# Performance work log

Hardware: AMD Instinct MI355X
Metric: run time of the kernel (lower is better)

Reference implementation:

```python
import jax, jax.numpy as jnp
import numpy as np

D_MODEL = 96
D_STATE = 6
D_CONV = 9
D_INNER = 2 * D_MODEL          # expand = 2
DT_RANK = (D_MODEL + 15) // 16  # ceil(d_model/16) = 6
DIM_IN = 64
DIM_OUT = 64
BATCH = 16
SEQLEN = 4096


def setup_inputs() -> dict:
    key = jax.random.key(0)
    ks = jax.random.split(key, 12)
    def s(k, shape, scale=0.02):
        return jax.random.normal(k, shape, jnp.float32) * scale
    return {
        "x": jax.random.normal(ks[0], (BATCH, SEQLEN, D_MODEL), jnp.float32),
        # Mamba block params
        "in_proj_w": s(ks[1], (2 * D_INNER, D_MODEL)),
        "conv_w": s(ks[2], (D_INNER, D_CONV), 0.1),   # depthwise conv kernel
        "conv_b": jnp.zeros((D_INNER,), jnp.float32),
        "x_proj_w": s(ks[3], (DT_RANK + 2 * D_STATE, D_INNER)),
        "dt_proj_w": s(ks[4], (D_INNER, DT_RANK), 0.1),
        "dt_proj_b": s(ks[5], (D_INNER,), 0.1),
        "A_log": jnp.log(jnp.tile(jnp.arange(1, D_STATE + 1, dtype=jnp.float32), (D_INNER, 1))),
        "D_param": jnp.ones((D_INNER,), jnp.float32),
        "out_proj_w": s(ks[6], (D_MODEL, D_INNER)),
        "norm_w": jnp.ones((D_MODEL,), jnp.float32),  # RMSNorm weight
        # heads
        "out_fc_w": s(ks[7], (DIM_IN, D_MODEL)),
        "out_fc_b": jnp.zeros((DIM_IN,), jnp.float32),
        "mu_w": s(ks[8], (DIM_OUT, DIM_IN)),
        "mu_b": jnp.zeros((DIM_OUT,), jnp.float32),
        "sigma_w": s(ks[9], (DIM_OUT, DIM_IN)),
        "sigma_b": jnp.zeros((DIM_OUT,), jnp.float32),
    }


def _mamba_block(x, in_proj_w, conv_w, conv_b, x_proj_w, dt_proj_w, dt_proj_b,
                 A_log, D_param, out_proj_w):
    Bsz = x.shape[0]
    xz = jnp.einsum('bld,ed->ble', x, in_proj_w)          # (B,L,2*ED)
    xs, z = jnp.split(xz, 2, axis=-1)
    # causal depthwise conv1d (torch pads d_conv-1 both sides then trims right)
    xt = xs.transpose(0, 2, 1)                            # (B,ED,L)
    kern = conv_w[:, None, :]                             # (ED,1,K)
    xc = jax.lax.conv_general_dilated(xt, kern, window_strides=(1,),
                                      padding=[(D_CONV - 1, 0)],
                                      feature_group_count=D_INNER)
    xc = (xc + conv_b[None, :, None]).transpose(0, 2, 1)  # (B,L,ED)
    xc = jax.nn.silu(xc)
    dbc = jnp.einsum('ble,fe->blf', xc, x_proj_w)         # (B,L,dt_rank+2N)
    delta_r = dbc[..., :DT_RANK]
    Bm = dbc[..., DT_RANK:DT_RANK + D_STATE]              # (B,L,N)
    Cm = dbc[..., DT_RANK + D_STATE:]                     # (B,L,N)
    delta = jax.nn.softplus(jnp.einsum('blr,er->ble', delta_r, dt_proj_w) + dt_proj_b)
    A = -jnp.exp(A_log)                                   # (ED,N)
    deltaA = jnp.exp(delta[..., None] * A)                # (B,L,ED,N)
    BX = (delta * xc)[..., None] * Bm[:, :, None, :]      # (B,L,ED,N)

    def step(h, inputs):
        dA, bx = inputs
        h = dA * h + bx
        return h, h

    h0 = jnp.zeros((Bsz, D_INNER, D_STATE), x.dtype)
    _, hs = jax.lax.scan(step, h0, (deltaA.swapaxes(0, 1), BX.swapaxes(0, 1)))
    y = jnp.einsum('lben,bln->ble', hs, Cm)               # (B,L,ED)
    y = y + D_param * xc
    y = y * jax.nn.silu(z)
    return jnp.einsum('ble,de->bld', y, out_proj_w)       # (B,L,D)


def reference(x, in_proj_w, conv_w, conv_b, x_proj_w, dt_proj_w, dt_proj_b,
              A_log, D_param, out_proj_w, norm_w,
              out_fc_w, out_fc_b, mu_w, mu_b, sigma_w, sigma_b):
    # residual block: x + mixer(RMSNorm(x))   (dropout is identity at eval)
    h = x * jax.lax.rsqrt(jnp.mean(x * x, axis=-1, keepdims=True) + 1e-5) * norm_w
    out = x + _mamba_block(h, in_proj_w, conv_w, conv_b, x_proj_w,
                           dt_proj_w, dt_proj_b, A_log, D_param, out_proj_w)
    e = out.mean(axis=1)                                  # (B,D)
    feat = jax.nn.elu(jnp.tanh(e @ out_fc_w.T + out_fc_b))
    mu = feat @ mu_w.T + mu_b
    sigma = jax.nn.elu(feat @ sigma_w.T + sigma_b) + 1.0 + 1e-14
    return (feat, mu, sigma)
```

## Files before the change

### kernel.cpp

```cpp
#include <hip/hip_runtime.h>
#include <math.h>

#define BATCH 16
#define SEQLEN 4096
#define D_MODEL 96
#define D_STATE 6
#define D_CONV 9
#define D_INNER 192
#define DT_RANK 6
#define NPOS (BATCH * SEQLEN)

#define NC2 128
#define CT2 (SEQLEN / NC2)
#define NSEG 16
#define CPS (NC2 / NSEG)

#define OFF_XS    0L
#define OFF_Z     (OFF_XS   + (long)NPOS * 96)
#define OFF_OUT4  (OFF_Z    + (long)NPOS * 96)
#define OFF_SEG   (OFF_OUT4 + (long)BATCH * NC2 * 5 * 192 * 4)
#define OFF_XPART (OFF_SEG  + (long)BATCH * NSEG * 5 * 192 * 4)
#define OFF_XPB   (OFF_XPART + (long)(NPOS / 32) * 96)
#define OFF_WB16  (OFF_XPB  + 18 * 96)

typedef short v8s __attribute__((ext_vector_type(8)));
typedef float v4f __attribute__((ext_vector_type(4)));

__device__ __forceinline__ float silu_fast(float v) {
    return __fdividef(v, 1.0f + __expf(-v));
}
__device__ __forceinline__ float softplus_fast(float v) {
    return (v > 20.0f) ? v : __logf(1.0f + __expf(v));
}
__device__ __forceinline__ float eluf(float v) {
    return (v > 0.0f) ? v : expm1f(v);
}
__device__ __forceinline__ unsigned int pack_bf16(float a, float b) {
    unsigned int ua = __float_as_uint(a), ub = __float_as_uint(b);
    ua += 0x7FFFu + ((ua >> 16) & 1u);
    ub += 0x7FFFu + ((ub >> 16) & 1u);
    return (ua >> 16) | (ub & 0xFFFF0000u);
}
__device__ __forceinline__ unsigned short bf16h(float v) {
    unsigned int u = __float_as_uint(v);
    u += 0x7FFFu + ((u >> 16) & 1u);
    return (unsigned short)(u >> 16);
}
__device__ __forceinline__ float bf2f(unsigned short h) {
    return __uint_as_float(((unsigned int)h) << 16);
}

#define K0_W (384 * 48)
#define K0_X (18 * 96)
__global__ __launch_bounds__(256) void k0_pack(
    const float* __restrict__ W, const float* __restrict__ x_proj_w,
    unsigned int* __restrict__ wb16, unsigned int* __restrict__ xpb)
{
    int i = blockIdx.x * 256 + threadIdx.x;
    if (i < K0_W) {
        const float2 wv = *(const float2*)&W[2 * i];
        wb16[i] = pack_bf16(wv.x, wv.y);
    } else if (i < K0_W + K0_X) {
        int j = i - K0_W;
        const float2 wv = *(const float2*)&x_proj_w[2 * j];
        xpb[j] = pack_bf16(wv.x, wv.y);
    }
}

#define TP1 32
__global__ __launch_bounds__(256, 4) void k1_rmsnorm_inproj(
    const float* __restrict__ x, const unsigned short* __restrict__ wb16,
    const float* __restrict__ norm_w,
    unsigned short* __restrict__ xs, unsigned short* __restrict__ z,
    float* __restrict__ xpart)
{
    __shared__ float hRow[TP1 * 100];
    __shared__ unsigned int s_hA[TP1 * 52];
    __shared__ float s_part[TP1][8];
    __shared__ float s_scale[TP1];

    const int tid = threadIdx.x;
    const long p0 = (long)blockIdx.x * TP1;

    {
        const float4* x4 = (const float4*)&x[p0 * 96];
        for (int i = tid; i < TP1 * 24; i += 256) {
            int p = i / 24, dq = i - p * 24;
            *(float4*)&hRow[p * 100 + dq * 4] = x4[i];
        }
    }
    __syncthreads();

    {
        int p = tid >> 3, g = tid & 7;
        float ss = 0.0f;
        for (int d = g; d < 96; d += 8) { float v = hRow[p * 100 + d]; ss += v * v; }
        s_part[p][g] = ss;
    }
    __syncthreads();

    if (tid < TP1) {
        float ss = 0.0f;
#pragma unroll
        for (int g = 0; g < 8; g++) ss += s_part[tid][g];
        s_scale[tid] = 1.0f / sqrtf(ss / 96.0f + 1e-5f);
    } else if (tid < TP1 + 96) {
        int d = tid - TP1;
        float s = 0.0f;
        for (int p = 0; p < TP1; p++) s += hRow[p * 100 + d];
        xpart[(long)blockIdx.x * 96 + d] = s;
    }
    __syncthreads();

    {
        const float2* nw2 = (const float2*)norm_w;
        for (int i = tid; i < TP1 * 48; i += 256) {
            int p = i / 48, dp = i - p * 48;
            float sc = s_scale[p];
            float2 nv = nw2[dp];
            float v0 = hRow[p * 100 + 2 * dp]     * sc * nv.x;
            float v1 = hRow[p * 100 + 2 * dp + 1] * sc * nv.y;
            s_hA[p * 52 + dp] = pack_bf16(v0, v1);
        }
    }
    __syncthreads();

    const int wave = tid >> 6, lane = tid & 63;
    const int quad = lane >> 4, ln = lane & 15;
    const int n0 = wave * 96;

    v4f acc[2][6];
#pragma unroll
    for (int mt = 0; mt < 2; mt++)
#pragma unroll
        for (int nt = 0; nt < 6; nt++) acc[mt][nt] = (v4f){0.f, 0.f, 0.f, 0.f};

    for (int kc = 0; kc < 3; kc++) {
        v8s bfh[2];
#pragma unroll
        for (int mt = 0; mt < 2; mt++)
            bfh[mt] = *(const v8s*)&s_hA[(mt * 16 + ln) * 52 + kc * 16 + quad * 4];
#pragma unroll
        for (int nt = 0; nt < 6; nt++) {
            v8s aw = *(const v8s*)&wb16[(n0 + nt * 16 + ln) * 96 + kc * 32 + quad * 8];
            acc[0][nt] = __builtin_amdgcn_mfma_f32_16x16x32_bf16(aw, bfh[0], acc[0][nt], 0, 0, 0);
            acc[1][nt] = __builtin_amdgcn_mfma_f32_16x16x32_bf16(aw, bfh[1], acc[1][nt], 0, 0, 0);
        }
    }

    unsigned short* dst = (wave < 2) ? xs : z;
    const bool is_z = (wave >= 2);
    const int jb = (wave & 1) * 96;
#pragma unroll
    for (int mt = 0; mt < 2; mt++) {
        long pos = p0 + mt * 16 + ln;
#pragma unroll
        for (int nt = 0; nt < 6; nt++) {
            float f0 = acc[mt][nt][0], f1 = acc[mt][nt][1];
            float f2 = acc[mt][nt][2], f3 = acc[mt][nt][3];
            if (is_z) {
                f0 = silu_fast(f0); f1 = silu_fast(f1);
                f2 = silu_fast(f2); f3 = silu_fast(f3);
            }
            uint2 v;
            v.x = pack_bf16(f0, f1);
            v.y = pack_bf16(f2, f3);
            *(uint2*)&dst[pos * D_INNER + jb + nt * 16 + quad * 4] = v;
        }
    }
}

#define SXSTR 200
__global__ __launch_bounds__(192, 4) void k2f_conv_scan(
    const unsigned short* __restrict__ xs, const unsigned short* __restrict__ z,
    const float* __restrict__ conv_w, const float* __restrict__ conv_b,
    const unsigned short* __restrict__ xpb,
    const float* __restrict__ dt_w, const float* __restrict__ dt_b,
    const float* __restrict__ A_log, const float* __restrict__ D_param,
    float4* __restrict__ out4)
{
    __shared__ unsigned short sxc[CT2 * SXSTR];
    __shared__ float sMeta[CT2][20];
    const int e = threadIdx.x;
    const int c = blockIdx.x & (NC2 - 1);
    const int b = blockIdx.x >> 7;
    const int l0 = c * CT2;
    const long brow = (long)b * SEQLEN;

    float cw[D_CONV];
#pragma unroll
    for (int k = 0; k < D_CONV; k++) cw[k] = conv_w[e * D_CONV + k];
    const float cb = conv_b[e];
    float win[D_CONV];
#pragma unroll
    for (int k = 0; k < 8; k++) {
        int ll = l0 - 8 + k;
        win[k] = (ll >= 0) ? bf2f(xs[(brow + ll) * D_INNER + e]) : 0.0f;
    }
#pragma unroll
    for (int r = 0; r < CT2; r++) {
        win[8] = bf2f(xs[(brow + l0 + r) * D_INNER + e]);
        float s = cb;
#pragma unroll
        for (int k = 0; k < D_CONV; k++) s += win[k] * cw[k];
        sxc[r * SXSTR + e] = bf16h(silu_fast(s));
#pragma unroll
        for (int k = 0; k < 8; k++) win[k] = win[k + 1];
    }

    const unsigned short* zp = &z[(brow + l0) * D_INNER + e];
    float zv[CT2];
#pragma unroll
    for (int t = 0; t < CT2; t++) zv[t] = bf2f(zp[(long)t * D_INNER]);
    __syncthreads();

    {
        const int wave = e >> 6, lane = e & 63;
        const int quad = lane >> 4, ln = lane & 15;
        if (wave < 2) {
            const int mt = wave;
            const int r1 = (ln < 2) ? 16 + ln : 0;
            v4f dacc[2];
            dacc[0] = (v4f){0.f, 0.f, 0.f, 0.f};
            dacc[1] = (v4f){0.f, 0.f, 0.f, 0.f};
#pragma unroll
            for (int kc = 0; kc < 6; kc++) {
                v8s af  = *(const v8s*)&sxc[(mt * 16 + ln) * SXSTR + kc * 32 + quad * 8];
                v8s bf0 = *(const v8s*)&xpb[ln * 192 + kc * 32 + quad * 8];
                v8s bf1 = *(const v8s*)&xpb[r1 * 192 + kc * 32 + quad * 8];
                dacc[0] = __builtin_amdgcn_mfma_f32_16x16x32_bf16(af, bf0, dacc[0], 0, 0, 0);
                dacc[1] = __builtin_amdgcn_mfma_f32_16x16x32_bf16(af, bf1, dacc[1], 0, 0, 0);
            }
#pragma unroll
            for (int nt = 0; nt < 2; nt++) {
                int f = nt * 16 + ln;
                if (f < 18) {
                    int col = (f < 6) ? f : f + 2;
#pragma unroll
                    for (int r = 0; r < 4; r++)
                        sMeta[mt * 16 + quad * 4 + r][col] = dacc[nt][r];
                }
            }
        }
    }
    __syncthreads();

    float a[D_STATE];
#pragma unroll
    for (int n = 0; n < D_STATE; n++) a[n] = -__expf(A_log[e * D_STATE + n]);
    float dtw[DT_RANK];
#pragma unroll
    for (int q = 0; q < DT_RANK; q++) dtw[q] = dt_w[e * DT_RANK + q];
    const float dtb = dt_b[e];
    const float Dv = D_param[e];
    const float a0 = a[0];

    bool pok = true;
#pragma unroll
    for (int n = 1; n < D_STATE; n++)
        pok = pok && (fabsf(a[n] - (float)(n + 1) * a0)
                      <= 1e-4f * (float)(n + 1) * fabsf(a0));
    unsigned long long pmask = __ballot(pok);

    float S[D_STATE], G[D_STATE];
#pragma unroll
    for (int n = 0; n < D_STATE; n++) { S[n] = 0.0f; G[n] = 0.0f; }
    float ysum0 = 0.0f;

    if (pmask == 0xFFFFFFFFFFFFFFFFull) {
        float Pa = 1.0f;
#pragma unroll 2
        for (int t = 0; t < CT2; t++) {
            const float4* m4 = (const float4*)&sMeta[t][0];
            float4 m0 = m4[0], m1 = m4[1], mB0 = m4[2], mB1 = m4[3], mC = m4[4];
            float Bv[6] = {mB0.x, mB0.y, mB0.z, mB0.w, mB1.x, mB1.y};
            float Cv[6] = {mB1.z, mB1.w, mC.x, mC.y, mC.z, mC.w};
            float dr = dtb + m0.x * dtw[0] + m0.y * dtw[1] + m0.z * dtw[2]
                     + m0.w * dtw[3] + m1.x * dtw[4] + m1.y * dtw[5];
            float dl = softplus_fast(dr);
            float xv = bf2f(sxc[t * SXSTR + e]);
            float zw = zv[t];
            float dx = dl * xv;
            float y = Dv * xv;
            float E = __expf(dl * a0);
            Pa *= E;
            float dA = E;
            float w = zw * Pa;
#pragma unroll
            for (int n = 0; n < D_STATE; n++) {
                S[n] = dA * S[n] + dx * Bv[n];
                y += S[n] * Cv[n];
                G[n] += w * Cv[n];
                dA *= E;
                w *= Pa;
            }
            ysum0 += zw * y;
        }
        long ob = (long)(b * NC2 + c) * 5 * 192 + e;
        float P1 = Pa, P2 = P1 * Pa, P3 = P2 * Pa, P4 = P3 * Pa, P5 = P4 * Pa, P6 = P5 * Pa;
        float4 q0, q1, q2, q3, q4;
        q0.x=P1; q0.y=P2; q0.z=P3; q0.w=P4;
        q1.x=P5; q1.y=P6; q1.z=S[0]; q1.w=S[1];
        q2.x=S[2]; q2.y=S[3]; q2.z=S[4]; q2.w=S[5];
        q3.x=G[0]; q3.y=G[1]; q3.z=G[2]; q3.w=G[3];
        q4.x=G[4]; q4.y=G[5]; q4.z=ysum0; q4.w=0.0f;
        out4[ob          ] = q0;
        out4[ob + 192    ] = q1;
        out4[ob + 2 * 192] = q2;
        out4[ob + 3 * 192] = q3;
        out4[ob + 4 * 192] = q4;
    } else {
        float P[D_STATE];
#pragma unroll
        for (int n = 0; n < D_STATE; n++) P[n] = 1.0f;
#pragma unroll 2
        for (int t = 0; t < CT2; t++) {
            const float4* m4 = (const float4*)&sMeta[t][0];
            float4 m0 = m4[0], m1 = m4[1], mB0 = m4[2], mB1 = m4[3], mC = m4[4];
            float Bv[6] = {mB0.x, mB0.y, mB0.z, mB0.w, mB1.x, mB1.y};
            float Cv[6] = {mB1.z, mB1.w, mC.x, mC.y, mC.z, mC.w};
            float dr = dtb + m0.x * dtw[0] + m0.y * dtw[1] + m0.z * dtw[2]
                     + m0.w * dtw[3] + m1.x * dtw[4] + m1.y * dtw[5];
            float dl = softplus_fast(dr);
            float xv = bf2f(sxc[t * SXSTR + e]);
            float zw = zv[t];
            float dx = dl * xv;
            float y = Dv * xv;
#pragma unroll
            for (int n = 0; n < D_STATE; n++) {
                float dA = __expf(dl * a[n]);
                S[n] = dA * S[n] + dx * Bv[n];
                P[n] *= dA;
                y += S[n] * Cv[n];
                G[n] += zw * P[n] * Cv[n];
            }
            ysum0 += zw * y;
        }
        long ob = (long)(b * NC2 + c) * 5 * 192 + e;
        float4 q0, q1, q2, q3, q4;
        q0.x=P[0]; q0.y=P[1]; q0.z=P[2]; q0.w=P[3];
        q1.x=P[4]; q1.y=P[5]; q1.z=S[0]; q1.w=S[1];
        q2.x=S[2]; q2.y=S[3]; q2.z=S[4]; q2.w=S[5];
        q3.x=G[0]; q3.y=G[1]; q3.z=G[2]; q3.w=G[3];
        q4.x=G[4]; q4.y=G[5]; q4.z=ysum0; q4.w=0.0f;
        out4[ob          ] = q0;
        out4[ob + 192    ] = q1;
        out4[ob + 2 * 192] = q2;
        out4[ob + 3 * 192] = q3;
        out4[ob + 4 * 192] = q4;
    }
}

__global__ __launch_bounds__(192) void k4_seg(
    const float4* __restrict__ out4, float4* __restrict__ seg4)
{
    const int e = threadIdx.x;
    const int s = blockIdx.x & (NSEG - 1);
    const int b = blockIdx.x >> 4;

    float H[D_STATE], Gq[D_STATE], Pp[D_STATE];
#pragma unroll
    for (int n = 0; n < D_STATE; n++) { H[n] = 0.0f; Gq[n] = 0.0f; Pp[n] = 1.0f; }
    float yb = 0.0f;
#pragma unroll 2
    for (int cc = 0; cc < CPS; cc++) {
        int c = s * CPS + cc;
        long ob = (long)(b * NC2 + c) * 5 * 192 + e;
        float4 q0 = out4[ob];
        float4 q1 = out4[ob + 192];
        float4 q2 = out4[ob + 2 * 192];
        float4 q3 = out4[ob + 3 * 192];
        float4 q4 = out4[ob + 4 * 192];
        float Pv[6] = {q0.x, q0.y, q0.z, q0.w, q1.x, q1.y};
        float Sv[6] = {q1.z, q1.w, q2.x, q2.y, q2.z, q2.w};
        float Gv[6] = {q3.x, q3.y, q3.z, q3.w, q4.x, q4.y};
        float g = 0.0f;
#pragma unroll
        for (int n = 0; n < D_STATE; n++) g += Gv[n] * H[n];
        yb += q4.z + g;
#pragma unroll
        for (int n = 0; n < D_STATE; n++) {
            Gq[n] += Gv[n] * Pp[n];
            H[n] = Pv[n] * H[n] + Sv[n];
            Pp[n] *= Pv[n];
        }
    }
    long sb = (long)(b * NSEG + s) * 5 * 192 + e;
    float4 q0, q1, q2, q3, q4;
    q0.x=Pp[0]; q0.y=Pp[1]; q0.z=Pp[2]; q0.w=Pp[3];
    q1.x=Pp[4]; q1.y=Pp[5]; q1.z=H[0]; q1.w=H[1];
    q2.x=H[2]; q2.y=H[3]; q2.z=H[4]; q2.w=H[5];
    q3.x=Gq[0]; q3.y=Gq[1]; q3.z=Gq[2]; q3.w=Gq[3];
    q4.x=Gq[4]; q4.y=Gq[5]; q4.z=yb; q4.w=0.0f;
    seg4[sb          ] = q0;
    seg4[sb + 192    ] = q1;
    seg4[sb + 2 * 192] = q2;
    seg4[sb + 3 * 192] = q3;
    seg4[sb + 4 * 192] = q4;
}

__global__ __launch_bounds__(192) void k4_head(
    const float4* __restrict__ seg4, const float* __restrict__ xpart,
    const float* __restrict__ Wout,
    const float* __restrict__ fc_w, const float* __restrict__ fc_b,
    const float* __restrict__ mu_w, const float* __restrict__ mu_b,
    const float* __restrict__ sg_w, const float* __restrict__ sg_b,
    float* __restrict__ out)
{
    __shared__ float ybar[D_INNER];
    __shared__ float sxb[D_MODEL];
    __shared__ float evec[D_MODEL];
    __shared__ float feat_s[64];
    const int e = threadIdx.x;
    const int b = blockIdx.x;

    float H[D_STATE];
#pragma unroll
    for (int n = 0; n < D_STATE; n++) H[n] = 0.0f;
    float yb = 0.0f;
#pragma unroll 4
    for (int s = 0; s < NSEG; s++) {
        long ob = (long)(b * NSEG + s) * 5 * 192 + e;
        float4 q0 = seg4[ob];
        float4 q1 = seg4[ob + 192];
        float4 q2 = seg4[ob + 2 * 192];
        float4 q3 = seg4[ob + 3 * 192];
        float4 q4 = seg4[ob + 4 * 192];
        float Pv[6] = {q0.x, q0.y, q0.z, q0.w, q1.x, q1.y};
        float Sv[6] = {q1.z, q1.w, q2.x, q2.y, q2.z, q2.w};
        float Gv[6] = {q3.x, q3.y, q3.z, q3.w, q4.x, q4.y};
        float g = 0.0f;
#pragma unroll
        for (int n = 0; n < D_STATE; n++) g += Gv[n] * H[n];
        yb += q4.z + g;
#pragma unroll
        for (int n = 0; n < D_STATE; n++) H[n] = Pv[n] * H[n] + Sv[n];
    }
    ybar[e] = yb;

    if (e < D_MODEL) {
        const float* xp = &xpart[(long)b * 128 * 96 + e];
        float s = 0.0f;
        for (int t = 0; t < 128; t++) s += xp[t * 96];
        sxb[e] = s;
    }
    __syncthreads();

    if (e < D_MODEL) {
        float s = sxb[e];
        const float* wrow = &Wout[e * D_INNER];
        for (int e2 = 0; e2 < D_INNER; e2++) s += ybar[e2] * wrow[e2];
        evec[e] = s / (float)SEQLEN;
    }
    __syncthreads();

    if (e < 64) {
        float s = fc_b[e];
        const float* wrow = &fc_w[e * D_MODEL];
        for (int d = 0; d < D_MODEL; d++) s += evec[d] * wrow[d];
        float f = eluf(tanhf(s));
        feat_s[e] = f;
        out[b * 64 + e] = f;
    }
    __syncthreads();

    if (e < 64) {
        float smu = mu_b[e], ssg = sg_b[e];
        const float* mrow = &mu_w[e * 64];
        const float* srow = &sg_w[e * 64];
        for (int i = 0; i < 64; i++) {
            smu += feat_s[i] * mrow[i];
            ssg += feat_s[i] * srow[i];
        }
        out[1024 + b * 64 + e] = smu;
        out[2048 + b * 64 + e] = eluf(ssg) + 1.0f + 1e-14f;
    }
}

extern "C" void kernel_launch(void* const* d_in, const int* in_sizes, int n_in,
                              void* d_out, int out_size, void* d_ws, size_t ws_size,
                              hipStream_t stream) {
    const float* x         = (const float*)d_in[0];
    const float* in_proj_w = (const float*)d_in[1];
    const float* conv_w    = (const float*)d_in[2];
    const float* conv_b    = (const float*)d_in[3];
    const float* x_proj_w  = (const float*)d_in[4];
    const float* dt_proj_w = (const float*)d_in[5];
    const float* dt_proj_b = (const float*)d_in[6];
    const float* A_log     = (const float*)d_in[7];
    const float* D_param   = (const float*)d_in[8];
    const float* out_proj_w= (const float*)d_in[9];
    const float* norm_w    = (const float*)d_in[10];
    const float* out_fc_w  = (const float*)d_in[11];
    const float* out_fc_b  = (const float*)d_in[12];
    const float* mu_w      = (const float*)d_in[13];
    const float* mu_b      = (const float*)d_in[14];
    const float* sigma_w   = (const float*)d_in[15];
    const float* sigma_b   = (const float*)d_in[16];
    float* ws = (float*)d_ws;
    float* out = (float*)d_out;

    k0_pack<<<(K0_W + K0_X + 255) / 256, 256, 0, stream>>>(
        in_proj_w, x_proj_w,
        (unsigned int*)(ws + OFF_WB16), (unsigned int*)(ws + OFF_XPB));

    k1_rmsnorm_inproj<<<NPOS / TP1, 256, 0, stream>>>(
        x, (const unsigned short*)(ws + OFF_WB16), norm_w,
        (unsigned short*)(ws + OFF_XS), (unsigned short*)(ws + OFF_Z),
        ws + OFF_XPART);

    k2f_conv_scan<<<BATCH * NC2, 192, 0, stream>>>(
        (const unsigned short*)(ws + OFF_XS), (const unsigned short*)(ws + OFF_Z),
        conv_w, conv_b, (const unsigned short*)(ws + OFF_XPB),
        dt_proj_w, dt_proj_b, A_log, D_param,
        (float4*)(ws + OFF_OUT4));

    k4_seg<<<BATCH * NSEG, 192, 0, stream>>>(
        (const float4*)(ws + OFF_OUT4), (float4*)(ws + OFF_SEG));

    k4_head<<<BATCH, 192, 0, stream>>>(
        (const float4*)(ws + OFF_SEG), ws + OFF_XPART, out_proj_w,
        out_fc_w, out_fc_b, mu_w, mu_b, sigma_w, sigma_b, out);
}
```

Before: 195.1 us.

## Split conv+x_proj GEMM out of scan kernel into separate pre-pass kernel

Moves the depthwise causal conv, SiLU and x_proj MFMA GEMM out of the fused scan kernel into a new kernel that processes 64-position tiles and writes xc (bf16) and the dt/B/C projections (fp32) to workspace. The scan kernel then only loads these precomputed tiles into shared memory before the chunked scan. This shortens the per-block prologue of the scan kernel and removes its conv halo recompute. In exchange it adds an extra kernel launch and a global round trip for xc and the projection values.

```diff
diff --git a/kernel.cpp b/kernel.cpp
--- a/kernel.cpp
+++ b/kernel.cpp
@@ -22,6 +22,8 @@
 #define OFF_XPART (OFF_SEG  + (long)BATCH * NSEG * 5 * 192 * 4)
 #define OFF_XPB   (OFF_XPART + (long)(NPOS / 32) * 96)
 #define OFF_WB16  (OFF_XPB  + 18 * 96)
+#define OFF_XC    (OFF_WB16 + 384 * 48)
+#define OFF_DBC   (OFF_XC   + (long)NPOS * 96)
 
 typedef short v8s __attribute__((ext_vector_type(8)));
 typedef float v4f __attribute__((ext_vector_type(4)));
@@ -171,10 +173,81 @@
 }
 
 #define SXSTR 200
-__global__ __launch_bounds__(192, 4) void k2f_conv_scan(
-    const unsigned short* __restrict__ xs, const unsigned short* __restrict__ z,
+#define CVP 64
+__global__ __launch_bounds__(192, 4) void k15_convgemm(
+    const unsigned short* __restrict__ xs,
     const float* __restrict__ conv_w, const float* __restrict__ conv_b,
     const unsigned short* __restrict__ xpb,
+    unsigned short* __restrict__ xc, float* __restrict__ dbcw)
+{
+    __shared__ unsigned short sxk[CVP * SXSTR];
+    const int e = threadIdx.x;
+    const int s = blockIdx.x & 63;
+    const int b = blockIdx.x >> 6;
+    const int l0 = s * CVP;
+    const long brow = (long)b * SEQLEN;
+
+    float cw[D_CONV];
+#pragma unroll
+    for (int k = 0; k < D_CONV; k++) cw[k] = conv_w[e * D_CONV + k];
+    const float cb = conv_b[e];
+    float win[D_CONV];
+#pragma unroll
+    for (int k = 0; k < 8; k++) {
+        int ll = l0 - 8 + k;
+        win[k] = (ll >= 0) ? bf2f(xs[(brow + ll) * D_INNER + e]) : 0.0f;
+    }
+    const unsigned short* xp = &xs[(brow + l0) * D_INNER + e];
+    unsigned short* cp = &xc[(brow + l0) * D_INNER + e];
+#pragma unroll 8
+    for (int r = 0; r < CVP; r++) {
+        win[8] = bf2f(xp[(long)r * D_INNER]);
+        float sa = cb;
+#pragma unroll
+        for (int k = 0; k < D_CONV; k++) sa += win[k] * cw[k];
+        unsigned short h = bf16h(silu_fast(sa));
+        sxk[r * SXSTR + e] = h;
+        cp[(long)r * D_INNER] = h;
+#pragma unroll
+        for (int k = 0; k < 8; k++) win[k] = win[k + 1];
+    }
+    __syncthreads();
+
+    const int wave = e >> 6, lane = e & 63;
+    const int quad = lane >> 4, ln = lane & 15;
+    if (wave < 2) {
+        const int r1 = (ln < 2) ? 16 + ln : 0;
+#pragma unroll
+        for (int half = 0; half < 2; half++) {
+            const int mt = wave * 2 + half;
+            v4f dacc[2];
+            dacc[0] = (v4f){0.f, 0.f, 0.f, 0.f};
+            dacc[1] = (v4f){0.f, 0.f, 0.f, 0.f};
+#pragma unroll
+            for (int kc = 0; kc < 6; kc++) {
+                v8s af  = *(const v8s*)&sxk[(mt * 16 + ln) * SXSTR + kc * 32 + quad * 8];
+                v8s bf0 = *(const v8s*)&xpb[ln * 192 + kc * 32 + quad * 8];
+                v8s bf1 = *(const v8s*)&xpb[r1 * 192 + kc * 32 + quad * 8];
+                dacc[0] = __builtin_amdgcn_mfma_f32_16x16x32_bf16(af, bf0, dacc[0], 0, 0, 0);
+                dacc[1] = __builtin_amdgcn_mfma_f32_16x16x32_bf16(af, bf1, dacc[1], 0, 0, 0);
+            }
+#pragma unroll
+            for (int nt = 0; nt < 2; nt++) {
+                int f = nt * 16 + ln;
+                if (f < 18) {
+                    int col = (f < 6) ? f : f + 2;
+#pragma unroll
+                    for (int r = 0; r < 4; r++)
+                        dbcw[(brow + l0 + mt * 16 + quad * 4 + r) * 20 + col] = dacc[nt][r];
+                }
+            }
+        }
+    }
+}
+
+__global__ __launch_bounds__(192, 4) void k2s_scan(
+    const unsigned short* __restrict__ xc, const unsigned short* __restrict__ z,
+    const float* __restrict__ dbcw,
     const float* __restrict__ dt_w, const float* __restrict__ dt_b,
     const float* __restrict__ A_log, const float* __restrict__ D_param,
     float4* __restrict__ out4)
@@ -187,62 +260,25 @@
     const int l0 = c * CT2;
     const long brow = (long)b * SEQLEN;
 
-    float cw[D_CONV];
-#pragma unroll
-    for (int k = 0; k < D_CONV; k++) cw[k] = conv_w[e * D_CONV + k];
-    const float cb = conv_b[e];
-    float win[D_CONV];
-#pragma unroll
-    for (int k = 0; k < 8; k++) {
-        int ll = l0 - 8 + k;
-        win[k] = (ll >= 0) ? bf2f(xs[(brow + ll) * D_INNER + e]) : 0.0f;
-    }
-#pragma unroll
-    for (int r = 0; r < CT2; r++) {
-        win[8] = bf2f(xs[(brow + l0 + r) * D_INNER + e]);
-        float s = cb;
-#pragma unroll
-        for (int k = 0; k < D_CONV; k++) s += win[k] * cw[k];
-        sxc[r * SXSTR + e] = bf16h(silu_fast(s));
-#pragma unroll
-        for (int k = 0; k < 8; k++) win[k] = win[k + 1];
-    }
-
+    if (e < 160) {
+        int t = e / 5, q = e - t * 5;
+        *(float4*)&sMeta[t][q * 4] =
+            *(const float4*)&dbcw[(brow + l0 + t) * 20 + q * 4];
+    }
+    {
+        const unsigned short* src = &xc[(brow + l0) * D_INNER];
+#pragma unroll
+        for (int j = 0; j < 4; j++) {
+            int i = e + j * 192;
+            int row = i / 24, c8 = i - row * 24;
+            *(v8s*)&sxc[row * SXSTR + c8 * 8] =
+                *(const v8s*)&src[row * D_INNER + c8 * 8];
+        }
+    }
     const unsigned short* zp = &z[(brow + l0) * D_INNER + e];
     float zv[CT2];
 #pragma unroll
     for (int t = 0; t < CT2; t++) zv[t] = bf2f(zp[(long)t * D_INNER]);
-    __syncthreads();
-
-    {
-        const int wave = e >> 6, lane = e & 63;
-        const int quad = lane >> 4, ln = lane & 15;
-        if (wave < 2) {
-            const int mt = wave;
-            const int r1 = (ln < 2) ? 16 + ln : 0;
-            v4f dacc[2];
-            dacc[0] = (v4f){0.f, 0.f, 0.f, 0.f};
-            dacc[1] = (v4f){0.f, 0.f, 0.f, 0.f};
-#pragma unroll
-            for (int kc = 0; kc < 6; kc++) {
-                v8s af  = *(const v8s*)&sxc[(mt * 16 + ln) * SXSTR + kc * 32 + quad * 8];
-                v8s bf0 = *(const v8s*)&xpb[ln * 192 + kc * 32 + quad * 8];
-                v8s bf1 = *(const v8s*)&xpb[r1 * 192 + kc * 32 + quad * 8];
-                dacc[0] = __builtin_amdgcn_mfma_f32_16x16x32_bf16(af, bf0, dacc[0], 0, 0, 0);
-                dacc[1] = __builtin_amdgcn_mfma_f32_16x16x32_bf16(af, bf1, dacc[1], 0, 0, 0);
-            }
-#pragma unroll
-            for (int nt = 0; nt < 2; nt++) {
-                int f = nt * 16 + ln;
-                if (f < 18) {
-                    int col = (f < 6) ? f : f + 2;
-#pragma unroll
-                    for (int r = 0; r < 4; r++)
-                        sMeta[mt * 16 + quad * 4 + r][col] = dacc[nt][r];
-                }
-            }
-        }
-    }
     __syncthreads();
 
     float a[D_STATE];
@@ -509,9 +545,14 @@
         (unsigned short*)(ws + OFF_XS), (unsigned short*)(ws + OFF_Z),
         ws + OFF_XPART);
 
-    k2f_conv_scan<<<BATCH * NC2, 192, 0, stream>>>(
-        (const unsigned short*)(ws + OFF_XS), (const unsigned short*)(ws + OFF_Z),
-        conv_w, conv_b, (const unsigned short*)(ws + OFF_XPB),
+    k15_convgemm<<<BATCH * (SEQLEN / CVP), 192, 0, stream>>>(
+        (const unsigned short*)(ws + OFF_XS), conv_w, conv_b,
+        (const unsigned short*)(ws + OFF_XPB),
+        (unsigned short*)(ws + OFF_XC), ws + OFF_DBC);
+
+    k2s_scan<<<BATCH * NC2, 192, 0, stream>>>(
+        (const unsigned short*)(ws + OFF_XC), (const unsigned short*)(ws + OFF_Z),
+        ws + OFF_DBC,
         dt_proj_w, dt_proj_b, A_log, D_param,
         (float4*)(ws + OFF_OUT4));
 
```

After: 202.1 us. +3.6%, slower.

## Process two scan chunks per block with interleaved independent recurrences

Applied to the files above, without the earlier changes.

Each conv/scan block now handles two adjacent chunks instead of one, halving the grid. The two chunks' scan recurrences are interleaved in one loop to expose instruction-level parallelism across independent dependency chains. The conv window is shared across the chunks, which removes a redundant halo reload. The z values for both chunks are packed as bf16 pairs into one register array. In exchange it uses more registers and shared memory per block and launches fewer blocks, which may reduce occupancy or load balance.

```diff
diff --git a/kernel.cpp b/kernel.cpp
--- a/kernel.cpp
+++ b/kernel.cpp
@@ -12,6 +12,7 @@
 
 #define NC2 128
 #define CT2 (SEQLEN / NC2)
+#define CPB 2
 #define NSEG 16
 #define CPS (NC2 / NSEG)
 
@@ -179,12 +180,13 @@
     const float* __restrict__ A_log, const float* __restrict__ D_param,
     float4* __restrict__ out4)
 {
-    __shared__ unsigned short sxc[CT2 * SXSTR];
-    __shared__ float sMeta[CT2][20];
+    __shared__ unsigned short sxc[CPB * CT2 * SXSTR];
+    __shared__ float sMeta[CPB * CT2][20];
     const int e = threadIdx.x;
-    const int c = blockIdx.x & (NC2 - 1);
-    const int b = blockIdx.x >> 7;
-    const int l0 = c * CT2;
+    const int cidx = blockIdx.x & (NC2 / CPB - 1);
+    const int b = blockIdx.x >> 6;
+    const int c0 = cidx * CPB;
+    const int l0 = c0 * CT2;
     const long brow = (long)b * SEQLEN;
 
     float cw[D_CONV];
@@ -197,9 +199,10 @@
         int ll = l0 - 8 + k;
         win[k] = (ll >= 0) ? bf2f(xs[(brow + ll) * D_INNER + e]) : 0.0f;
     }
-#pragma unroll
-    for (int r = 0; r < CT2; r++) {
-        win[8] = bf2f(xs[(brow + l0 + r) * D_INNER + e]);
+    const unsigned short* xsp = &xs[(brow + l0) * D_INNER + e];
+#pragma unroll 8
+    for (int r = 0; r < CPB * CT2; r++) {
+        win[8] = bf2f(xsp[(long)r * D_INNER]);
         float s = cb;
 #pragma unroll
         for (int k = 0; k < D_CONV; k++) s += win[k] * cw[k];
@@ -209,36 +212,43 @@
     }
 
     const unsigned short* zp = &z[(brow + l0) * D_INNER + e];
-    float zv[CT2];
-#pragma unroll
-    for (int t = 0; t < CT2; t++) zv[t] = bf2f(zp[(long)t * D_INNER]);
+    unsigned int zq[CT2];
+#pragma unroll
+    for (int t = 0; t < CT2; t++) {
+        unsigned int lo = zp[(long)t * D_INNER];
+        unsigned int hi = zp[(long)(t + CT2) * D_INNER];
+        zq[t] = lo | (hi << 16);
+    }
     __syncthreads();
 
     {
         const int wave = e >> 6, lane = e & 63;
         const int quad = lane >> 4, ln = lane & 15;
         if (wave < 2) {
-            const int mt = wave;
             const int r1 = (ln < 2) ? 16 + ln : 0;
-            v4f dacc[2];
-            dacc[0] = (v4f){0.f, 0.f, 0.f, 0.f};
-            dacc[1] = (v4f){0.f, 0.f, 0.f, 0.f};
-#pragma unroll
-            for (int kc = 0; kc < 6; kc++) {
-                v8s af  = *(const v8s*)&sxc[(mt * 16 + ln) * SXSTR + kc * 32 + quad * 8];
-                v8s bf0 = *(const v8s*)&xpb[ln * 192 + kc * 32 + quad * 8];
-                v8s bf1 = *(const v8s*)&xpb[r1 * 192 + kc * 32 + quad * 8];
-                dacc[0] = __builtin_amdgcn_mfma_f32_16x16x32_bf16(af, bf0, dacc[0], 0, 0, 0);
-                dacc[1] = __builtin_amdgcn_mfma_f32_16x16x32_bf16(af, bf1, dacc[1], 0, 0, 0);
-            }
-#pragma unroll
-            for (int nt = 0; nt < 2; nt++) {
-                int f = nt * 16 + ln;
-                if (f < 18) {
-                    int col = (f < 6) ? f : f + 2;
-#pragma unroll
-                    for (int r = 0; r < 4; r++)
-                        sMeta[mt * 16 + quad * 4 + r][col] = dacc[nt][r];
+#pragma unroll
+            for (int half = 0; half < 2; half++) {
+                const int mt = wave * 2 + half;
+                v4f dacc[2];
+                dacc[0] = (v4f){0.f, 0.f, 0.f, 0.f};
+                dacc[1] = (v4f){0.f, 0.f, 0.f, 0.f};
+#pragma unroll
+                for (int kc = 0; kc < 6; kc++) {
+                    v8s af  = *(const v8s*)&sxc[(mt * 16 + ln) * SXSTR + kc * 32 + quad * 8];
+                    v8s bf0 = *(const v8s*)&xpb[ln * 192 + kc * 32 + quad * 8];
+                    v8s bf1 = *(const v8s*)&xpb[r1 * 192 + kc * 32 + quad * 8];
+                    dacc[0] = __builtin_amdgcn_mfma_f32_16x16x32_bf16(af, bf0, dacc[0], 0, 0, 0);
+                    dacc[1] = __builtin_amdgcn_mfma_f32_16x16x32_bf16(af, bf1, dacc[1], 0, 0, 0);
+                }
+#pragma unroll
+                for (int nt = 0; nt < 2; nt++) {
+                    int f = nt * 16 + ln;
+                    if (f < 18) {
+                        int col = (f < 6) ? f : f + 2;
+#pragma unroll
+                        for (int r = 0; r < 4; r++)
+                            sMeta[mt * 16 + quad * 4 + r][col] = dacc[nt][r];
+                    }
                 }
             }
         }
@@ -262,92 +272,141 @@
                       <= 1e-4f * (float)(n + 1) * fabsf(a0));
     unsigned long long pmask = __ballot(pok);
 
-    float S[D_STATE], G[D_STATE];
-#pragma unroll
-    for (int n = 0; n < D_STATE; n++) { S[n] = 0.0f; G[n] = 0.0f; }
-    float ysum0 = 0.0f;
-
     if (pmask == 0xFFFFFFFFFFFFFFFFull) {
-        float Pa = 1.0f;
-#pragma unroll 2
+        float SA[D_STATE], GA[D_STATE], SB[D_STATE], GB[D_STATE];
+#pragma unroll
+        for (int n = 0; n < D_STATE; n++) {
+            SA[n] = 0.0f; GA[n] = 0.0f; SB[n] = 0.0f; GB[n] = 0.0f;
+        }
+        float PaA = 1.0f, PaB = 1.0f, ysA = 0.0f, ysB = 0.0f;
         for (int t = 0; t < CT2; t++) {
-            const float4* m4 = (const float4*)&sMeta[t][0];
-            float4 m0 = m4[0], m1 = m4[1], mB0 = m4[2], mB1 = m4[3], mC = m4[4];
-            float Bv[6] = {mB0.x, mB0.y, mB0.z, mB0.w, mB1.x, mB1.y};
-            float Cv[6] = {mB1.z, mB1.w, mC.x, mC.y, mC.z, mC.w};
-            float dr = dtb + m0.x * dtw[0] + m0.y * dtw[1] + m0.z * dtw[2]
-                     + m0.w * dtw[3] + m1.x * dtw[4] + m1.y * dtw[5];
-            float dl = softplus_fast(dr);
-            float xv = bf2f(sxc[t * SXSTR + e]);
-            float zw = zv[t];
-            float dx = dl * xv;
-            float y = Dv * xv;
-            float E = __expf(dl * a0);
-            Pa *= E;
-            float dA = E;
-            float w = zw * Pa;
-#pragma unroll
-            for (int n = 0; n < D_STATE; n++) {
-                S[n] = dA * S[n] + dx * Bv[n];
-                y += S[n] * Cv[n];
-                G[n] += w * Cv[n];
-                dA *= E;
-                w *= Pa;
+            {
+                const float4* m4 = (const float4*)&sMeta[t][0];
+                float4 m0 = m4[0], m1 = m4[1], mB0 = m4[2], mB1 = m4[3], mC = m4[4];
+                float Bv[6] = {mB0.x, mB0.y, mB0.z, mB0.w, mB1.x, mB1.y};
+                float Cv[6] = {mB1.z, mB1.w, mC.x, mC.y, mC.z, mC.w};
+                float dr = dtb + m0.x * dtw[0] + m0.y * dtw[1] + m0.z * dtw[2]
+                         + m0.w * dtw[3] + m1.x * dtw[4] + m1.y * dtw[5];
+                float dl = softplus_fast(dr);
+                float xv = bf2f(sxc[t * SXSTR + e]);
+                float zw = __uint_as_float(zq[t] << 16);
+                float dx = dl * xv;
+                float y = Dv * xv;
+                float E = __expf(dl * a0);
+                PaA *= E;
+                float dA = E;
+                float w = zw * PaA;
+#pragma unroll
+                for (int n = 0; n < D_STATE; n++) {
+                    SA[n] = dA * SA[n] + dx * Bv[n];
+                    y += SA[n] * Cv[n];
+                    GA[n] += w * Cv[n];
+                    dA *= E;
+                    w *= PaA;
+                }
+                ysA += zw * y;
             }
-            ysum0 += zw * y;
-        }
-        long ob = (long)(b * NC2 + c) * 5 * 192 + e;
-        float P1 = Pa, P2 = P1 * Pa, P3 = P2 * Pa, P4 = P3 * Pa, P5 = P4 * Pa, P6 = P5 * Pa;
-        float4 q0, q1, q2, q3, q4;
-        q0.x=P1; q0.y=P2; q0.z=P3; q0.w=P4;
-        q1.x=P5; q1.y=P6; q1.z=S[0]; q1.w=S[1];
-        q2.x=S[2]; q2.y=S[3]; q2.z=S[4]; q2.w=S[5];
-        q3.x=G[0]; q3.y=G[1]; q3.z=G[2]; q3.w=G[3];
-        q4.x=G[4]; q4.y=G[5]; q4.z=ysum0; q4.w=0.0f;
-        out4[ob          ] = q0;
-        out4[ob + 192    ] = q1;
-        out4[ob + 2 * 192] = q2;
-        out4[ob + 3 * 192] = q3;
-        out4[ob + 4 * 192] = q4;
+            {
+                const float4* m4 = (const float4*)&sMeta[CT2 + t][0];
+                float4 m0 = m4[0], m1 = m4[1], mB0 = m4[2], mB1 = m4[3], mC = m4[4];
+                float Bv[6] = {mB0.x, mB0.y, mB0.z, mB0.w, mB1.x, mB1.y};
+                float Cv[6] = {mB1.z, mB1.w, mC.x, mC.y, mC.z, mC.w};
+                float dr = dtb + m0.x * dtw[0] + m0.y * dtw[1] + m0.z * dtw[2]
+                         + m0.w * dtw[3] + m1.x * dtw[4] + m1.y * dtw[5];
+                float dl = softplus_fast(dr);
+                float xv = bf2f(sxc[(CT2 + t) * SXSTR + e]);
+                float zw = __uint_as_float(zq[t] & 0xFFFF0000u);
+                float dx = dl * xv;
+                float y = Dv * xv;
+                float E = __expf(dl * a0);
+                PaB *= E;
+                float dA = E;
+                float w = zw * PaB;
+#pragma unroll
+                for (int n = 0; n < D_STATE; n++) {
+                    SB[n] = dA * SB[n] + dx * Bv[n];
+                    y += SB[n] * Cv[n];
+                    GB[n] += w * Cv[n];
+                    dA *= E;
+                    w *= PaB;
+                }
+                ysB += zw * y;
+            }
+        }
+        {
+            long ob = (long)(b * NC2 + c0) * 5 * 192 + e;
+            float Pa = PaA;
+            float P1 = Pa, P2 = P1 * Pa, P3 = P2 * Pa, P4 = P3 * Pa, P5 = P4 * Pa, P6 = P5 * Pa;
+            float4 q0, q1, q2, q3, q4;
+            q0.x=P1; q0.y=P2; q0.z=P3; q0.w=P4;
+            q1.x=P5; q1.y=P6; q1.z=SA[0]; q1.w=SA[1];
+            q2.x=SA[2]; q2.y=SA[3]; q2.z=SA[4]; q2.w=SA[5];
+            q3.x=GA[0]; q3.y=GA[1]; q3.z=GA[2]; q3.w=GA[3];
+            q4.x=GA[4]; q4.y=GA[5]; q4.z=ysA; q4.w=0.0f;
+            out4[ob          ] = q0;
+            out4[ob + 192    ] = q1;
+            out4[ob + 2 * 192] = q2;
+            out4[ob + 3 * 192] = q3;
+            out4[ob + 4 * 192] = q4;
+        }
+        {
+            long ob = (long)(b * NC2 + c0 + 1) * 5 * 192 + e;
+            float Pa = PaB;
+            float P1 = Pa, P2 = P1 * Pa, P3 = P2 * Pa, P4 = P3 * Pa, P5 = P4 * Pa, P6 = P5 * Pa;
+            float4 q0, q1, q2, q3, q4;
+            q0.x=P1; q0.y=P2; q0.z=P3; q0.w=P4;
+            q1.x=P5; q1.y=P6; q1.z=SB[0]; q1.w=SB[1];
+            q2.x=SB[2]; q2.y=SB[3]; q2.z=SB[4]; q2.w=SB[5];
+            q3.x=GB[0]; q3.y=GB[1]; q3.z=GB[2]; q3.w=GB[3];
+            q4.x=GB[4]; q4.y=GB[5]; q4.z=ysB; q4.w=0.0f;
+            out4[ob          ] = q0;
+            out4[ob + 192    ] = q1;
+            out4[ob + 2 * 192] = q2;
+            out4[ob + 3 * 192] = q3;
+            out4[ob + 4 * 192] = q4;
+        }
     } else {
-        float P[D_STATE];
-#pragma unroll
-        for (int n = 0; n < D_STATE; n++) P[n] = 1.0f;
-#pragma unroll 2
-        for (int t = 0; t < CT2; t++) {
-            const float4* m4 = (const float4*)&sMeta[t][0];
-            float4 m0 = m4[0], m1 = m4[1], mB0 = m4[2], mB1 = m4[3], mC = m4[4];
-            float Bv[6] = {mB0.x, mB0.y, mB0.z, mB0.w, mB1.x, mB1.y};
-            float Cv[6] = {mB1.z, mB1.w, mC.x, mC.y, mC.z, mC.w};
-            float dr = dtb + m0.x * dtw[0] + m0.y * dtw[1] + m0.z * dtw[2]
-                     + m0.w * dtw[3] + m1.x * dtw[4] + m1.y * dtw[5];
-            float dl = softplus_fast(dr);
-            float xv = bf2f(sxc[t * SXSTR + e]);
-            float zw = zv[t];
-            float dx = dl * xv;
-            float y = Dv * xv;
-#pragma unroll
-            for (int n = 0; n < D_STATE; n++) {
-                float dA = __expf(dl * a[n]);
-                S[n] = dA * S[n] + dx * Bv[n];
-                P[n] *= dA;
-                y += S[n] * Cv[n];
-                G[n] += zw * P[n] * Cv[n];
+        for (int cc = 0; cc < CPB; cc++) {
+            float S[D_STATE], G[D_STATE], P[D_STATE];
+#pragma unroll
+            for (int n = 0; n < D_STATE; n++) { S[n] = 0.0f; G[n] = 0.0f; P[n] = 1.0f; }
+            float ysum0 = 0.0f;
+            for (int t = 0; t < CT2; t++) {
+                const float4* m4 = (const float4*)&sMeta[cc * CT2 + t][0];
+                float4 m0 = m4[0], m1 = m4[1], mB0 = m4[2], mB1 = m4[3], mC = m4[4];
+                float Bv[6] = {mB0.x, mB0.y, mB0.z, mB0.w, mB1.x, mB1.y};
+                float Cv[6] = {mB1.z, mB1.w, mC.x, mC.y, mC.z, mC.w};
+                float dr = dtb + m0.x * dtw[0] + m0.y * dtw[1] + m0.z * dtw[2]
+                         + m0.w * dtw[3] + m1.x * dtw[4] + m1.y * dtw[5];
+                float dl = softplus_fast(dr);
+                float xv = bf2f(sxc[(cc * CT2 + t) * SXSTR + e]);
+                float zw = (cc == 0) ? __uint_as_float(zq[t] << 16)
+                                     : __uint_as_float(zq[t] & 0xFFFF0000u);
+                float dx = dl * xv;
+                float y = Dv * xv;
+#pragma unroll
+                for (int n = 0; n < D_STATE; n++) {
+                    float dA = __expf(dl * a[n]);
+                    S[n] = dA * S[n] + dx * Bv[n];
+                    P[n] *= dA;
+                    y += S[n] * Cv[n];
+                    G[n] += zw * P[n] * Cv[n];
+                }
+                ysum0 += zw * y;
             }
-            ysum0 += zw * y;
-        }
-        long ob = (long)(b * NC2 + c) * 5 * 192 + e;
-        float4 q0, q1, q2, q3, q4;
-        q0.x=P[0]; q0.y=P[1]; q0.z=P[2]; q0.w=P[3];
-        q1.x=P[4]; q1.y=P[5]; q1.z=S[0]; q1.w=S[1];
-        q2.x=S[2]; q2.y=S[3]; q2.z=S[4]; q2.w=S[5];
-        q3.x=G[0]; q3.y=G[1]; q3.z=G[2]; q3.w=G[3];
-        q4.x=G[4]; q4.y=G[5]; q4.z=ysum0; q4.w=0.0f;
-        out4[ob          ] = q0;
-        out4[ob + 192    ] = q1;
-        out4[ob + 2 * 192] = q2;
-        out4[ob + 3 * 192] = q3;
-        out4[ob + 4 * 192] = q4;
+            long ob = (long)(b * NC2 + c0 + cc) * 5 * 192 + e;
+            float4 q0, q1, q2, q3, q4;
+            q0.x=P[0]; q0.y=P[1]; q0.z=P[2]; q0.w=P[3];
+            q1.x=P[4]; q1.y=P[5]; q1.z=S[0]; q1.w=S[1];
+            q2.x=S[2]; q2.y=S[3]; q2.z=S[4]; q2.w=S[5];
+            q3.x=G[0]; q3.y=G[1]; q3.z=G[2]; q3.w=G[3];
+            q4.x=G[4]; q4.y=G[5]; q4.z=ysum0; q4.w=0.0f;
+            out4[ob          ] = q0;
+            out4[ob + 192    ] = q1;
+            out4[ob + 2 * 192] = q2;
+            out4[ob + 3 * 192] = q3;
+            out4[ob + 4 * 192] = q4;
+        }
     }
 }
 
@@ -509,7 +568,7 @@
         (unsigned short*)(ws + OFF_XS), (unsigned short*)(ws + OFF_Z),
         ws + OFF_XPART);
 
-    k2f_conv_scan<<<BATCH * NC2, 192, 0, stream>>>(
+    k2f_conv_scan<<<BATCH * NC2 / CPB, 192, 0, stream>>>(
         (const unsigned short*)(ws + OFF_XS), (const unsigned short*)(ws + OFF_Z),
         conv_w, conv_b, (const unsigned short*)(ws + OFF_XPB),
         dt_proj_w, dt_proj_b, A_log, D_param,
```

New measurement: 207.3 us. +6.3%, slower.
